# Kernel optimization log

Measured on AMD Instinct MI355X. Metric: run time of the kernel, lower is better.

Reference implementation:

```python
import jax, jax.numpy as jnp
import numpy as np

N = 65536          # nodes
E = N * 7          # edges (avg_degree = n_edge_type = 7)
C_IN = 128
C_OUT = 128
N_EDGE_TYPE = 7
N_NODE_TYPE = 5
FEAT = C_IN + N_NODE_TYPE  # 133, channels after one-hot concat


def setup_inputs() -> dict:
    key = jax.random.key(0)
    k1, k2, k3, k4, k5 = jax.random.split(key, 5)
    x = jax.random.normal(k1, (N, C_IN), dtype=jnp.float32)
    edge_idx = jax.random.randint(k2, (2, E), 0, N, dtype=jnp.int64)
    edge_type = jax.random.randint(k3, (E,), 0, N_EDGE_TYPE, dtype=jnp.int64)
    node_type = jax.random.randint(k4, (N,), 0, N_NODE_TYPE, dtype=jnp.int64)
    # uniform init a la module's reset_parameters
    fan_in = 7 * C_IN
    fan_out = 7 * C_OUT
    a = np.sqrt(3.0) * np.sqrt(2.0 / (fan_in + fan_out))
    weights = jax.random.uniform(k5, (N_EDGE_TYPE * FEAT, C_OUT), dtype=jnp.float32,
                                 minval=-a, maxval=a)
    return {"x": x, "edge_idx": edge_idx, "edge_type": edge_type,
            "node_type": node_type, "weights": weights}


def reference(x, edge_idx, edge_type, node_type, weights):
    # one-hot node type concat (n_node_type > 1 branch)
    one_hot = jax.nn.one_hot(node_type, N_NODE_TYPE, dtype=x.dtype)
    xa = jnp.concatenate([x, one_hot], axis=1)          # [N, FEAT]
    row, col = edge_idx[0], edge_idx[1]
    seg = row * N_EDGE_TYPE + edge_type                 # [E]
    gathered = xa[col]                                  # [E, FEAT]
    num_seg = N * N_EDGE_TYPE
    sums = jax.ops.segment_sum(gathered, seg, num_segments=num_seg)
    cnt = jax.ops.segment_sum(jnp.ones((E,), dtype=xa.dtype), seg, num_segments=num_seg)
    col_data = sums / jnp.maximum(cnt, 1.0)[:, None]    # scatter_mean
    # overwrite self-loop slot (last edge type) with node's own features
    self_idx = jnp.arange(N, dtype=jnp.int64) * N_EDGE_TYPE + (N_EDGE_TYPE - 1)
    col_data = col_data.at[self_idx].set(xa)
    out = col_data.reshape(N, N_EDGE_TYPE * FEAT) @ weights  # [N, C_OUT]
    return out
```

## Files before the change

### kernel.cpp

```cpp
#include <hip/hip_runtime.h>
#include <hip/hip_bf16.h>

#define N_NODES 65536
#define N_EDGES (N_NODES * 7)
#define NSEG    (N_NODES * 7)
#define CAP     12

typedef short short8 __attribute__((ext_vector_type(8)));
typedef float f32x4  __attribute__((ext_vector_type(4)));

__device__ __forceinline__ unsigned short f2bf(float f) {
    unsigned u = __float_as_uint(f);
    unsigned r = (u + 0x7FFFu + ((u >> 16) & 1u)) >> 16;
    return (unsigned short)r;
}
__device__ __forceinline__ unsigned pack2(float lo, float hi) {
    return (unsigned)f2bf(lo) | ((unsigned)f2bf(hi) << 16);
}
__device__ __forceinline__ float bflo(unsigned d) { return __uint_as_float(d << 16); }
__device__ __forceinline__ float bfhi(unsigned d) { return __uint_as_float(d & 0xffff0000u); }

__global__ __launch_bounds__(256) void k_big(const float* __restrict__ x,
                                             const int* __restrict__ eidx,
                                             const int* __restrict__ etype,
                                             const int* __restrict__ ntype,
                                             const float* __restrict__ W,
                                             unsigned short* __restrict__ xb,
                                             unsigned short* __restrict__ wb,
                                             unsigned long long* __restrict__ seg64,
                                             unsigned short* __restrict__ scol) {
    int i = blockIdx.x * 256 + threadIdx.x;

    if (i < N_EDGES) {
        int t = etype[i];
        if (t < 6) {
            int r = eidx[i];
            int c = eidx[N_EDGES + i];
            int u = ntype[c];
            unsigned seg = (unsigned)r * 7u + (unsigned)t;
            unsigned long long inc = 1ull | (1ull << (8 + 10 * u));
            unsigned long long old = atomicAdd(&seg64[seg], inc);
            unsigned slot = (unsigned)(old & 0xffull);
            if (slot < CAP) scol[seg * CAP + slot] = (unsigned short)c;
        }
    }

    {
        int row = i >> 4, mm = i & 15;
        const f32x4* p = reinterpret_cast<const f32x4*>(x + (size_t)row * 128 + mm * 8);
        f32x4 v0 = p[0], v1 = p[1];
        uint4 w;
        w.x = pack2(v0[0], v0[1]); w.y = pack2(v0[2], v0[3]);
        w.z = pack2(v1[0], v1[1]); w.w = pack2(v1[2], v1[3]);
        reinterpret_cast<uint4*>(xb)[i] = w;
    }

    if (i < 143360) {
        int j    = i & 7;
        int lane = (i >> 3) & 63;
        int cb   = (i >> 9) & 7;
        int tkc  = i >> 12;
        int kc   = tkc % 5;
        int t    = tkc / 5;
        int k = kc * 32 + ((lane >> 4) << 3) + j;
        int c = cb * 16 + (lane & 15);
        float v = (k < 133) ? W[(t * 133 + k) * 128 + c] : 0.0f;
        wb[i] = f2bf(v);
    }
}

__global__ __launch_bounds__(512, 4) void k_main(const unsigned short* __restrict__ xb,
                                                 const int* __restrict__ ntype,
                                                 const unsigned long long* __restrict__ seg64,
                                                 const unsigned short* __restrict__ scol,
                                                 const unsigned short* __restrict__ wb,
                                                 float* __restrict__ out) {
    __shared__ unsigned short sA[7 * 32 * 168];

    const int tid  = threadIdx.x;
    const int lane = tid & 63;
    const int wid  = tid >> 6;
    const int n0   = blockIdx.x * 32;
    const int r    = tid >> 4;
    const int m    = tid & 15;
    const int n    = n0 + r;

    for (int i = tid; i < 7 * 32 * 12; i += 512) {
        int row = i / 12, j = i - row * 12;
        reinterpret_cast<unsigned*>(sA)[row * 84 + 68 + j] = 0u;
    }

    unsigned vlo = 0u, vhi = 0u;
    if (m < 7) {
        uint2 v = reinterpret_cast<const uint2*>(seg64)[n * 7 + m];
        vlo = v.x; vhi = v.y;
    }
    unsigned clo[6], chi[6], c_t[6];
    #pragma unroll
    for (int t = 0; t < 6; ++t) {
        clo[t] = (unsigned)__shfl((int)vlo, (lane & 48) + t);
        chi[t] = (unsigned)__shfl((int)vhi, (lane & 48) + t);
        c_t[t] = clo[t] & 0xffu;
    }

    uint2 q2[6];
    #pragma unroll
    for (int t = 0; t < 6; ++t)
        q2[t] = *reinterpret_cast<const uint2*>(scol + ((size_t)n * 7 + t) * CAP);

    short8 xA[6], xB[6], xS;
    #pragma unroll
    for (int t = 0; t < 6; ++t) {
        unsigned cA = (c_t[t] >= 1u) ? (q2[t].x & 0xffffu) : (unsigned)n;
        unsigned cB = (c_t[t] >= 2u) ? (q2[t].x >> 16)     : (unsigned)n;
        xA[t] = *reinterpret_cast<const short8*>(xb + (size_t)cA * 128 + m * 8);
        xB[t] = *reinterpret_cast<const short8*>(xb + (size_t)cB * 128 + m * 8);
    }
    xS = *reinterpret_cast<const short8*>(xb + (size_t)n * 128 + m * 8);
    const int ntS = ntype[n];

    #pragma unroll
    for (int t = 0; t < 6; ++t) {
        const unsigned cntv = c_t[t];
        const float inv = (cntv > 1u) ? __builtin_amdgcn_rcpf((float)cntv) : 1.0f;

        uint4 a4 = *reinterpret_cast<const uint4*>(&xA[t]);
        uint4 b4 = *reinterpret_cast<const uint4*>(&xB[t]);
        a4.x = (cntv >= 1u) ? a4.x : 0u; a4.y = (cntv >= 1u) ? a4.y : 0u;
        a4.z = (cntv >= 1u) ? a4.z : 0u; a4.w = (cntv >= 1u) ? a4.w : 0u;
        b4.x = (cntv >= 2u) ? b4.x : 0u; b4.y = (cntv >= 2u) ? b4.y : 0u;
        b4.z = (cntv >= 2u) ? b4.z : 0u; b4.w = (cntv >= 2u) ? b4.w : 0u;

        float a[8];
        a[0] = bflo(a4.x) + bflo(b4.x); a[1] = bfhi(a4.x) + bfhi(b4.x);
        a[2] = bflo(a4.y) + bflo(b4.y); a[3] = bfhi(a4.y) + bfhi(b4.y);
        a[4] = bflo(a4.z) + bflo(b4.z); a[5] = bfhi(a4.z) + bfhi(b4.z);
        a[6] = bflo(a4.w) + bflo(b4.w); a[7] = bfhi(a4.w) + bfhi(b4.w);

        if (cntv >= 3u) {
            const unsigned ce = (cntv < (unsigned)CAP) ? cntv : (unsigned)CAP;
            {
                unsigned c2 = q2[t].y & 0xffffu;
                short8 v = *reinterpret_cast<const short8*>(xb + (size_t)c2 * 128 + m * 8);
                uint4 v4 = *reinterpret_cast<const uint4*>(&v);
                a[0] += bflo(v4.x); a[1] += bfhi(v4.x);
                a[2] += bflo(v4.y); a[3] += bfhi(v4.y);
                a[4] += bflo(v4.z); a[5] += bfhi(v4.z);
                a[6] += bflo(v4.w); a[7] += bfhi(v4.w);
            }
            if (ce >= 4u) {
                unsigned c3 = q2[t].y >> 16;
                short8 v = *reinterpret_cast<const short8*>(xb + (size_t)c3 * 128 + m * 8);
                uint4 v4 = *reinterpret_cast<const uint4*>(&v);
                a[0] += bflo(v4.x); a[1] += bfhi(v4.x);
                a[2] += bflo(v4.y); a[3] += bfhi(v4.y);
                a[4] += bflo(v4.z); a[5] += bfhi(v4.z);
                a[6] += bflo(v4.w); a[7] += bfhi(v4.w);
                const size_t segbase = ((size_t)n * 7 + t) * CAP;
                for (unsigned e = 4; e < ce; ++e) {
                    unsigned c = scol[segbase + e];
                    short8 ve = *reinterpret_cast<const short8*>(xb + (size_t)c * 128 + m * 8);
                    uint4 v4e = *reinterpret_cast<const uint4*>(&ve);
                    a[0] += bflo(v4e.x); a[1] += bfhi(v4e.x);
                    a[2] += bflo(v4e.y); a[3] += bfhi(v4e.y);
                    a[4] += bflo(v4e.z); a[5] += bfhi(v4e.z);
                    a[6] += bflo(v4e.w); a[7] += bfhi(v4e.w);
                }
            }
        }

        uint4 w;
        w.x = pack2(a[0] * inv, a[1] * inv); w.y = pack2(a[2] * inv, a[3] * inv);
        w.z = pack2(a[4] * inv, a[5] * inv); w.w = pack2(a[6] * inv, a[7] * inv);
        *reinterpret_cast<uint4*>(sA + (t * 32 + r) * 168 + m * 8) = w;

        if (m < 8) {
            unsigned long long v64 = ((unsigned long long)chi[t] << 32) | (unsigned long long)clo[t];
            float ohv = 0.0f;
            if (m < 5) ohv = (float)((unsigned)((v64 >> (8 + 10 * m)) & 0x3ffull)) * inv;
            sA[(t * 32 + r) * 168 + 128 + m] = f2bf(ohv);
        }
    }

    *reinterpret_cast<uint4*>(sA + (6 * 32 + r) * 168 + m * 8) =
        *reinterpret_cast<const uint4*>(&xS);
    if (m < 8)
        sA[(6 * 32 + r) * 168 + 128 + m] =
            (m == ntS) ? (unsigned short)0x3F80 : (unsigned short)0;

    short8 bv[2][5];
    #pragma unroll
    for (int kc = 0; kc < 5; ++kc)
        bv[0][kc] = *reinterpret_cast<const short8*>(
            wb + (((kc * 8 + wid) << 6) + lane) * 8);

    __syncthreads();

    f32x4 acc0 = {0.f, 0.f, 0.f, 0.f};
    f32x4 acc1 = {0.f, 0.f, 0.f, 0.f};
    const int ar = lane & 15;
    const int hi = (lane >> 4) << 3;

    #pragma unroll
    for (int t = 0; t < 7; ++t) {
        const int cur = t & 1, nxt = cur ^ 1;
        if (t < 6) {
            #pragma unroll
            for (int kc = 0; kc < 5; ++kc)
                bv[nxt][kc] = *reinterpret_cast<const short8*>(
                    wb + (((((t + 1) * 5 + kc) * 8 + wid) << 6) + lane) * 8);
        }
        #pragma unroll
        for (int kc = 0; kc < 5; ++kc) {
            short8 a0 = *reinterpret_cast<const short8*>(
                sA + (t * 32 + ar) * 168 + kc * 32 + hi);
            short8 a1 = *reinterpret_cast<const short8*>(
                sA + (t * 32 + 16 + ar) * 168 + kc * 32 + hi);
            acc0 = __builtin_amdgcn_mfma_f32_16x16x32_bf16(a0, bv[cur][kc], acc0, 0, 0, 0);
            acc1 = __builtin_amdgcn_mfma_f32_16x16x32_bf16(a1, bv[cur][kc], acc1, 0, 0, 0);
        }
    }

    const int orow = n0 + ((lane >> 4) << 2);
    const int ocol = (wid << 4) + (lane & 15);
    #pragma unroll
    for (int rr = 0; rr < 4; ++rr) {
        out[(size_t)(orow + rr) * 128 + ocol]      = acc0[rr];
        out[(size_t)(orow + 16 + rr) * 128 + ocol] = acc1[rr];
    }
}


extern "C" void kernel_launch(void* const* d_in, const int* in_sizes, int n_in,
                              void* d_out, int out_size, void* d_ws, size_t ws_size,
                              hipStream_t stream) {
    const float* x     = (const float*)d_in[0];
    const int*   eidx  = (const int*)d_in[1];
    const int*   etype = (const int*)d_in[2];
    const int*   ntype = (const int*)d_in[3];
    const float* W     = (const float*)d_in[4];
    float* out = (float*)d_out;

    unsigned short*     xb    = (unsigned short*)d_ws;
    unsigned short*     wb    = (unsigned short*)((char*)d_ws + 16777216);
    unsigned long long* seg64 = (unsigned long long*)((char*)d_ws + 17063936);
    unsigned short*     scol  = (unsigned short*)((char*)d_ws + 20733952);

    hipMemsetAsync(seg64, 0, NSEG * sizeof(unsigned long long), stream);
    k_big <<<4096,         256, 0, stream>>>(x, eidx, etype, ntype, W, xb, wb, seg64, scol);
    k_main<<<N_NODES / 32, 512, 0, stream>>>(xb, ntype, seg64, scol, wb, out);
}
```

Baseline: 84.25 us.

## Add zero row for empty segments, re-split MFMA waves, tweak bf16 and occupancy

Result: slower. 96.60 us (+14.7%).

```diff
diff --git a/kernel.cpp b/kernel.cpp
--- a/kernel.cpp
+++ b/kernel.cpp
@@ -5,14 +5,13 @@
 #define N_EDGES (N_NODES * 7)
 #define NSEG    (N_NODES * 7)
 #define CAP     12
+#define ZROW    65536
 
 typedef short short8 __attribute__((ext_vector_type(8)));
 typedef float f32x4  __attribute__((ext_vector_type(4)));
 
 __device__ __forceinline__ unsigned short f2bf(float f) {
-    unsigned u = __float_as_uint(f);
-    unsigned r = (u + 0x7FFFu + ((u >> 16) & 1u)) >> 16;
-    return (unsigned short)r;
+    return __builtin_bit_cast(unsigned short, (__bf16)f);
 }
 __device__ __forceinline__ unsigned pack2(float lo, float hi) {
     return (unsigned)f2bf(lo) | ((unsigned)f2bf(hi) << 16);
@@ -55,6 +54,8 @@
         reinterpret_cast<uint4*>(xb)[i] = w;
     }
 
+    if (i < 16) reinterpret_cast<uint4*>(xb + (size_t)ZROW * 128)[i] = (uint4){0u, 0u, 0u, 0u};
+
     if (i < 143360) {
         int j    = i & 7;
         int lane = (i >> 3) & 63;
@@ -69,7 +70,7 @@
     }
 }
 
-__global__ __launch_bounds__(512, 4) void k_main(const unsigned short* __restrict__ xb,
+__global__ __launch_bounds__(512, 2) void k_main(const unsigned short* __restrict__ xb,
                                                  const int* __restrict__ ntype,
                                                  const unsigned long long* __restrict__ seg64,
                                                  const unsigned short* __restrict__ scol,
@@ -90,29 +91,20 @@
         reinterpret_cast<unsigned*>(sA)[row * 84 + 68 + j] = 0u;
     }
 
-    unsigned vlo = 0u, vhi = 0u;
-    if (m < 7) {
-        uint2 v = reinterpret_cast<const uint2*>(seg64)[n * 7 + m];
-        vlo = v.x; vhi = v.y;
-    }
     unsigned clo[6], chi[6], c_t[6];
+    uint2 q2[6];
     #pragma unroll
     for (int t = 0; t < 6; ++t) {
-        clo[t] = (unsigned)__shfl((int)vlo, (lane & 48) + t);
-        chi[t] = (unsigned)__shfl((int)vhi, (lane & 48) + t);
-        c_t[t] = clo[t] & 0xffu;
-    }
-
-    uint2 q2[6];
-    #pragma unroll
-    for (int t = 0; t < 6; ++t)
+        uint2 v = reinterpret_cast<const uint2*>(seg64)[n * 7 + t];
+        clo[t] = v.x; chi[t] = v.y; c_t[t] = v.x & 0xffu;
         q2[t] = *reinterpret_cast<const uint2*>(scol + ((size_t)n * 7 + t) * CAP);
+    }
 
     short8 xA[6], xB[6], xS;
     #pragma unroll
     for (int t = 0; t < 6; ++t) {
-        unsigned cA = (c_t[t] >= 1u) ? (q2[t].x & 0xffffu) : (unsigned)n;
-        unsigned cB = (c_t[t] >= 2u) ? (q2[t].x >> 16)     : (unsigned)n;
+        unsigned cA = (c_t[t] >= 1u) ? (q2[t].x & 0xffffu) : (unsigned)ZROW;
+        unsigned cB = (c_t[t] >= 2u) ? (q2[t].x >> 16)     : (unsigned)ZROW;
         xA[t] = *reinterpret_cast<const short8*>(xb + (size_t)cA * 128 + m * 8);
         xB[t] = *reinterpret_cast<const short8*>(xb + (size_t)cB * 128 + m * 8);
     }
@@ -126,11 +118,6 @@
 
         uint4 a4 = *reinterpret_cast<const uint4*>(&xA[t]);
         uint4 b4 = *reinterpret_cast<const uint4*>(&xB[t]);
-        a4.x = (cntv >= 1u) ? a4.x : 0u; a4.y = (cntv >= 1u) ? a4.y : 0u;
-        a4.z = (cntv >= 1u) ? a4.z : 0u; a4.w = (cntv >= 1u) ? a4.w : 0u;
-        b4.x = (cntv >= 2u) ? b4.x : 0u; b4.y = (cntv >= 2u) ? b4.y : 0u;
-        b4.z = (cntv >= 2u) ? b4.z : 0u; b4.w = (cntv >= 2u) ? b4.w : 0u;
-
         float a[8];
         a[0] = bflo(a4.x) + bflo(b4.x); a[1] = bfhi(a4.x) + bfhi(b4.x);
         a[2] = bflo(a4.y) + bflo(b4.y); a[3] = bfhi(a4.y) + bfhi(b4.y);
@@ -174,59 +161,71 @@
         w.z = pack2(a[4] * inv, a[5] * inv); w.w = pack2(a[6] * inv, a[7] * inv);
         *reinterpret_cast<uint4*>(sA + (t * 32 + r) * 168 + m * 8) = w;
 
-        if (m < 8) {
+        if (m < 4) {
             unsigned long long v64 = ((unsigned long long)chi[t] << 32) | (unsigned long long)clo[t];
-            float ohv = 0.0f;
-            if (m < 5) ohv = (float)((unsigned)((v64 >> (8 + 10 * m)) & 0x3ffull)) * inv;
-            sA[(t * 32 + r) * 168 + 128 + m] = f2bf(ohv);
+            float g0 = 0.f, g1 = 0.f;
+            int i0 = 2 * m, i1 = 2 * m + 1;
+            if (i0 < 5) g0 = (float)((unsigned)((v64 >> (8 + 10 * i0)) & 0x3ffull));
+            if (i1 < 5) g1 = (float)((unsigned)((v64 >> (8 + 10 * i1)) & 0x3ffull));
+            reinterpret_cast<unsigned*>(sA)[(t * 32 + r) * 84 + 64 + m] =
+                pack2(g0 * inv, g1 * inv);
         }
     }
 
     *reinterpret_cast<uint4*>(sA + (6 * 32 + r) * 168 + m * 8) =
         *reinterpret_cast<const uint4*>(&xS);
-    if (m < 8)
-        sA[(6 * 32 + r) * 168 + 128 + m] =
-            (m == ntS) ? (unsigned short)0x3F80 : (unsigned short)0;
-
-    short8 bv[2][5];
-    #pragma unroll
-    for (int kc = 0; kc < 5; ++kc)
-        bv[0][kc] = *reinterpret_cast<const short8*>(
-            wb + (((kc * 8 + wid) << 6) + lane) * 8);
+    if (m < 4) {
+        float g0 = (ntS == 2 * m) ? 1.f : 0.f;
+        float g1 = (2 * m + 1 < 5 && ntS == 2 * m + 1) ? 1.f : 0.f;
+        reinterpret_cast<unsigned*>(sA)[(6 * 32 + r) * 84 + 64 + m] = pack2(g0, g1);
+    }
+
+    const int s  = wid & 1;
+    const int p  = wid >> 1;
+    const int ar = s * 16 + (lane & 15);
+    const int hi = (lane >> 4) << 3;
+
+    short8 bv[2][2][5];
+    #pragma unroll
+    for (int kc = 0; kc < 5; ++kc) {
+        bv[0][0][kc] = *reinterpret_cast<const short8*>(
+            wb + (((kc * 8 + 2 * p) << 6) + lane) * 8);
+        bv[0][1][kc] = *reinterpret_cast<const short8*>(
+            wb + (((kc * 8 + 2 * p + 1) << 6) + lane) * 8);
+    }
 
     __syncthreads();
 
     f32x4 acc0 = {0.f, 0.f, 0.f, 0.f};
     f32x4 acc1 = {0.f, 0.f, 0.f, 0.f};
-    const int ar = lane & 15;
-    const int hi = (lane >> 4) << 3;
 
     #pragma unroll
     for (int t = 0; t < 7; ++t) {
         const int cur = t & 1, nxt = cur ^ 1;
         if (t < 6) {
             #pragma unroll
-            for (int kc = 0; kc < 5; ++kc)
-                bv[nxt][kc] = *reinterpret_cast<const short8*>(
-                    wb + (((((t + 1) * 5 + kc) * 8 + wid) << 6) + lane) * 8);
+            for (int kc = 0; kc < 5; ++kc) {
+                bv[nxt][0][kc] = *reinterpret_cast<const short8*>(
+                    wb + (((((t + 1) * 5 + kc) * 8 + 2 * p) << 6) + lane) * 8);
+                bv[nxt][1][kc] = *reinterpret_cast<const short8*>(
+                    wb + (((((t + 1) * 5 + kc) * 8 + 2 * p + 1) << 6) + lane) * 8);
+            }
         }
         #pragma unroll
         for (int kc = 0; kc < 5; ++kc) {
-            short8 a0 = *reinterpret_cast<const short8*>(
+            short8 av = *reinterpret_cast<const short8*>(
                 sA + (t * 32 + ar) * 168 + kc * 32 + hi);
-            short8 a1 = *reinterpret_cast<const short8*>(
-                sA + (t * 32 + 16 + ar) * 168 + kc * 32 + hi);
-            acc0 = __builtin_amdgcn_mfma_f32_16x16x32_bf16(a0, bv[cur][kc], acc0, 0, 0, 0);
-            acc1 = __builtin_amdgcn_mfma_f32_16x16x32_bf16(a1, bv[cur][kc], acc1, 0, 0, 0);
-        }
-    }
-
-    const int orow = n0 + ((lane >> 4) << 2);
-    const int ocol = (wid << 4) + (lane & 15);
+            acc0 = __builtin_amdgcn_mfma_f32_16x16x32_bf16(av, bv[cur][0][kc], acc0, 0, 0, 0);
+            acc1 = __builtin_amdgcn_mfma_f32_16x16x32_bf16(av, bv[cur][1][kc], acc1, 0, 0, 0);
+        }
+    }
+
+    const int orow = n0 + s * 16 + ((lane >> 4) << 2);
+    const int ocol = (2 * p) * 16 + (lane & 15);
     #pragma unroll
     for (int rr = 0; rr < 4; ++rr) {
         out[(size_t)(orow + rr) * 128 + ocol]      = acc0[rr];
-        out[(size_t)(orow + 16 + rr) * 128 + ocol] = acc1[rr];
+        out[(size_t)(orow + rr) * 128 + ocol + 16] = acc1[rr];
     }
 }
 
@@ -242,9 +241,9 @@
     float* out = (float*)d_out;
 
     unsigned short*     xb    = (unsigned short*)d_ws;
-    unsigned short*     wb    = (unsigned short*)((char*)d_ws + 16777216);
-    unsigned long long* seg64 = (unsigned long long*)((char*)d_ws + 17063936);
-    unsigned short*     scol  = (unsigned short*)((char*)d_ws + 20733952);
+    unsigned short*     wb    = (unsigned short*)((char*)d_ws + 16777472);
+    unsigned long long* seg64 = (unsigned long long*)((char*)d_ws + 17064192);
+    unsigned short*     scol  = (unsigned short*)((char*)d_ws + 20734208);
 
     hipMemsetAsync(seg64, 0, NSEG * sizeof(unsigned long long), stream);
     k_big <<<4096,         256, 0, stream>>>(x, eidx, etype, ntype, W, xb, wb, seg64, scol);
```
